# Kernel tuning notes

Hardware: AMD Instinct MI355X
Metric: run time of the kernel (lower is better)

## Reference

```python
import jax, jax.numpy as jnp
import numpy as np

EPS = 1e-5

def _act_quant(x, bits=8):
    # per-token absmax quantization to signed int range, dequantized (STE)
    qb = float(2 ** (bits - 1) - 1)  # 127 for 8 bits
    scale = qb / jnp.clip(jnp.max(jnp.abs(x), axis=-1, keepdims=True), EPS, None)
    x_dq = jnp.clip(jnp.round(x * scale), -qb, qb) / scale
    return x + jax.lax.stop_gradient(x_dq - x)

def _weight_quant(w):
    # BitNet b1.58 ternary weights: scale = mean |W|, values in {-1,0,1} * scale (STE)
    s = jnp.clip(jnp.mean(jnp.abs(w)), EPS, None)
    w_dq = jnp.clip(jnp.round(w / s), -1.0, 1.0) * s
    return w + jax.lax.stop_gradient(w_dq - w)

def _bitlinear(x, w, bits=8):
    # x: [..., in], w: [out, in]
    return jnp.einsum('bsi,oi->bso', _act_quant(x, bits), _weight_quant(w))

def setup_inputs() -> dict:
    key = jax.random.key(0)
    k1, k2, k3 = jax.random.split(key, 3)
    B, S, H = 4, 4096, 2048
    I = int(H * 2.0)
    return {
        'hidden_states': jax.random.normal(k1, (B, S, H), dtype=jnp.float32),
        'w_up': jax.random.normal(k2, (I, H), dtype=jnp.float32) * (1.0 / np.sqrt(H)),
        'w_down': jax.random.normal(k3, (H, I), dtype=jnp.float32) * (1.0 / np.sqrt(I)),
    }

def reference(hidden_states, w_up, w_down):
    bits = 8
    h = _bitlinear(hidden_states, w_up, bits)          # [B,S,I]
    h = jnp.square(jax.nn.relu(h))                      # squared ReLU
    # dropout p=0.0 (eval) -> identity
    out = _bitlinear(h, w_down, bits)                   # [B,S,H]
    return out
```

## Files before the change

kernel.cpp:

```cpp
#include <hip/hip_runtime.h>
#include <hip/hip_bf16.h>

typedef signed char i8_t;
typedef _Float16 half_t;
typedef float v4fl __attribute__((ext_vector_type(4)));
typedef _Float16 v8h __attribute__((ext_vector_type(8)));
typedef int v4i __attribute__((ext_vector_type(4)));
typedef signed char v8c __attribute__((ext_vector_type(8)));
typedef signed char v16c __attribute__((ext_vector_type(16)));

__device__ __forceinline__ float ternqf(float w, float s) {
    float q = rintf(w / s);
    return fminf(1.f, fmaxf(-1.f, q));
}

__device__ __forceinline__ void gload16(const void* g, void* l) {
    __builtin_amdgcn_global_load_lds(
        (const __attribute__((address_space(1))) void*)g,
        (__attribute__((address_space(3))) void*)l, 16, 0, 0);
}

__global__ void abssum_partial2(const float* __restrict__ wup,
                                const float* __restrict__ wdn, long n,
                                float* __restrict__ part_up,
                                float* __restrict__ part_dn) {
    const int half = gridDim.x >> 1;
    const bool up = (blockIdx.x < half);
    const float* w = up ? wup : wdn;
    float* partial = up ? part_up : part_dn;
    const int bid = up ? blockIdx.x : blockIdx.x - half;
    long i0 = ((long)bid * 256 + threadIdx.x) * 8;
    long stride = (long)half * 256 * 8;
    float s = 0.f;
    for (long i = i0; i < n; i += stride) {
        v4fl a = *(const v4fl*)(w + i);
        v4fl b = *(const v4fl*)(w + i + 4);
#pragma unroll
        for (int j = 0; j < 4; ++j) s += fabsf(a[j]) + fabsf(b[j]);
    }
#pragma unroll
    for (int off = 32; off > 0; off >>= 1) s += __shfl_down(s, off, 64);
    __shared__ __align__(16) float red[4];
    if ((threadIdx.x & 63) == 0) red[threadIdx.x >> 6] = s;
    __syncthreads();
    if (threadIdx.x == 0)
        partial[bid] = (red[0] + red[1]) + (red[2] + red[3]);
}

__global__ void abssum_final(const float* __restrict__ part_up,
                             const float* __restrict__ part_dn,
                             float* __restrict__ scales, float inv) {
    const int wv = threadIdx.x >> 6;
    const int l = threadIdx.x & 63;
    const float* part = wv ? part_dn : part_up;
    float s = ((part[l] + part[l + 64]) + (part[l + 128] + part[l + 192]));
#pragma unroll
    for (int off = 32; off > 0; off >>= 1) s += __shfl_down(s, off, 64);
    if (l == 0) scales[wv] = fmaxf(s * inv, 1e-5f);
}

__global__ void wquant2_kernel(const float* __restrict__ wup,
                               const float* __restrict__ wdn,
                               i8_t* __restrict__ wqu, i8_t* __restrict__ wqd,
                               const float* __restrict__ scales, int wblocks) {
    const bool up = ((int)blockIdx.x < wblocks);
    const float* w = up ? wup : wdn;
    i8_t* wq = up ? wqu : wqd;
    const float s = up ? scales[0] : scales[1];
    const int bid = up ? blockIdx.x : blockIdx.x - wblocks;
    long i = ((long)bid * 256 + threadIdx.x) * 8;
    v4fl a = *(const v4fl*)(w + i);
    v4fl b = *(const v4fl*)(w + i + 4);
    v8c o;
#pragma unroll
    for (int j = 0; j < 4; ++j) {
        o[j]     = (i8_t)(int)ternqf(a[j], s);
        o[j + 4] = (i8_t)(int)ternqf(b[j], s);
    }
    *(v8c*)(wq + i) = o;
}

template <int W>
__global__ void rowquant_kernel(const float* __restrict__ src, i8_t* __restrict__ dst,
                                float* __restrict__ scale_out, int rows) {
    const int l = threadIdx.x & 63;
    const int row = blockIdx.x * 4 + (threadIdx.x >> 6);
    if (row >= rows) return;
    const int NI = W / 1024;
    const float* p = src + (size_t)row * W + l * 16;
    float v[NI * 16];
#pragma unroll
    for (int it = 0; it < NI; ++it) {
#pragma unroll
        for (int c = 0; c < 4; ++c) {
            v4fl a = *(const v4fl*)(p + it * 1024 + c * 4);
#pragma unroll
            for (int e = 0; e < 4; ++e) v[it * 16 + c * 4 + e] = a[e];
        }
    }
    float amax = 0.f;
#pragma unroll
    for (int j = 0; j < NI * 16; ++j) amax = fmaxf(amax, fabsf(v[j]));
#pragma unroll
    for (int off = 32; off > 0; off >>= 1)
        amax = fmaxf(amax, __shfl_xor(amax, off, 64));
    const float m = fmaxf(amax, 1e-5f);
    if (l == 0) scale_out[row] = m / 127.f;
    const float sc = 127.f / m;
    i8_t* q = dst + (size_t)row * W + l * 16;
#pragma unroll
    for (int it = 0; it < NI; ++it) {
        v16c o;
#pragma unroll
        for (int j = 0; j < 16; ++j) {
            float t = rintf(v[it * 16 + j] * sc);
            o[j] = (i8_t)(int)fminf(127.f, fmaxf(-127.f, t));
        }
        *(v16c*)(q + it * 1024) = o;
    }
}

template <typename T, int NV>
__global__ void hamax_kernel(const T* __restrict__ h, float* __restrict__ scale_out,
                             float* __restrict__ recip_out) {
    const int row = blockIdx.x;
    const int tid = threadIdx.x;
    const T* p = h + (size_t)row * (NV * 2048);
    float amax = 0.f;
#pragma unroll
    for (int it = 0; it < NV; ++it) {
        const T* s = p + ((size_t)it * 256 + tid) * 8;
#pragma unroll
        for (int j = 0; j < 8; ++j) amax = fmaxf(amax, fabsf((float)s[j]));
    }
#pragma unroll
    for (int off = 32; off > 0; off >>= 1) amax = fmaxf(amax, __shfl_xor(amax, off, 64));
    __shared__ __align__(16) float red[4];
    if ((tid & 63) == 0) red[tid >> 6] = amax;
    __syncthreads();
    if (tid == 0) {
        float m = fmaxf(fmaxf(red[0], red[1]), fmaxf(red[2], red[3]));
        m = fmaxf(m, 1e-5f);
        scale_out[row] = m / 127.f;
        recip_out[row] = 127.f / m;
    }
}

__device__ __forceinline__ void stage_tile256(const i8_t* __restrict__ g, int K,
                                              i8_t* l, int tid) {
#pragma unroll
    for (int i = 0; i < 4; ++i) {
        const int c = i * 512 + tid;
        const int r = c >> 3;
        const int lc = (((c & 7) ^ (r & 7)) << 4);
        gload16(g + (size_t)r * K + lc, l + c * 16);
    }
}

#define SB() __builtin_amdgcn_sched_barrier(0)

template <int EPI>
__launch_bounds__(512, 2)
__global__ void gemm_bt8(const i8_t* __restrict__ A, const i8_t* __restrict__ B,
                         void* __restrict__ Cv,
                         const float* __restrict__ rowscale,
                         const float* __restrict__ wscale,
                         int M, int N, int K) {
    __shared__ __align__(16) i8_t smem[131072];

    const int tid = threadIdx.x;

    const int gx = gridDim.x;
    const int nwg = gx * gridDim.y;
    int flat = blockIdx.y * gx + blockIdx.x;
    if ((nwg & 7) == 0) flat = (flat & 7) * (nwg >> 3) + (flat >> 3);
    const int n0 = (flat % gx) * 256;
    const int m0 = (flat / gx) * 256;

    const i8_t* gA = A + (size_t)m0 * K;
    const i8_t* gB = B + (size_t)n0 * K;

    const int w = tid >> 6, l = tid & 63;
    const int wr = w >> 2, wc = w & 3;
    const int lrow = l & 15, lq = l >> 4;
    const int lr7 = lrow & 7;
    const int kk0 = ((lq)     ^ lr7) << 4;
    const int kk1 = ((lq + 4) ^ lr7) << 4;
    const int aBase = ((wr * 128 + lrow) << 7);
    const int bBase = ((wc * 64 + lrow) << 7);

    v4i acc[8][4];
#pragma unroll
    for (int a = 0; a < 8; ++a)
#pragma unroll
        for (int b = 0; b < 4; ++b) acc[a][b] = (v4i){0, 0, 0, 0};

    const int NT = K >> 7;
    stage_tile256(gB, K, smem + 32768, tid);
    stage_tile256(gA, K, smem, tid);
    stage_tile256(gB + 128, K, smem + 65536 + 32768, tid);
    stage_tile256(gA + 128, K, smem + 65536, tid);
    asm volatile("s_waitcnt vmcnt(8)" ::: "memory");
    __builtin_amdgcn_s_barrier();
    SB();

    for (int t = 0; t < NT; ++t) {
        i8_t* Ab = smem + ((t & 1) << 16);
        i8_t* Bb = Ab + 32768;
        const bool pf = (t + 2 < NT);

        v4i a0[4], a1[4], b0[4], b1[4];

#pragma unroll
        for (int nj = 0; nj < 4; ++nj)
            b0[nj] = *(const v4i*)(Bb + bBase + (nj << 11) + kk0);
#pragma unroll
        for (int mi = 0; mi < 4; ++mi)
            a0[mi] = *(const v4i*)(Ab + aBase + (mi << 11) + kk0);
        SB();
#pragma unroll
        for (int nj = 0; nj < 4; ++nj)
            b1[nj] = *(const v4i*)(Bb + bBase + (nj << 11) + kk1);
#pragma unroll
        for (int mi = 0; mi < 4; ++mi)
            a1[mi] = *(const v4i*)(Ab + aBase + ((mi + 4) << 11) + kk0);
        SB();
        asm volatile("s_waitcnt lgkmcnt(8)" ::: "memory");
        SB();
        __builtin_amdgcn_s_setprio(1);
#pragma unroll
        for (int mi = 0; mi < 4; ++mi)
#pragma unroll
            for (int nj = 0; nj < 4; ++nj)
                acc[mi][nj] = __builtin_amdgcn_mfma_i32_16x16x64_i8(
                    a0[mi], b0[nj], acc[mi][nj], 0, 0, 0);
        __builtin_amdgcn_s_setprio(0);
        SB();
#pragma unroll
        for (int mi = 0; mi < 4; ++mi)
            a0[mi] = *(const v4i*)(Ab + aBase + (mi << 11) + kk1);
        SB();
        asm volatile("s_waitcnt lgkmcnt(4)" ::: "memory");
        SB();
        __builtin_amdgcn_s_setprio(1);
#pragma unroll
        for (int mi = 0; mi < 4; ++mi)
#pragma unroll
            for (int nj = 0; nj < 4; ++nj)
                acc[mi + 4][nj] = __builtin_amdgcn_mfma_i32_16x16x64_i8(
                    a1[mi], b0[nj], acc[mi + 4][nj], 0, 0, 0);
        __builtin_amdgcn_s_setprio(0);
        SB();
#pragma unroll
        for (int mi = 0; mi < 4; ++mi)
            a1[mi] = *(const v4i*)(Ab + aBase + ((mi + 4) << 11) + kk1);
        SB();
        asm volatile("s_waitcnt lgkmcnt(0)" ::: "memory");
        SB();
        __builtin_amdgcn_s_barrier();
        SB();
        if (pf) {
            stage_tile256(gB + (size_t)(t + 2) * 128, K, Bb, tid);
            stage_tile256(gA + (size_t)(t + 2) * 128, K, Ab, tid);
        }
        SB();
        __builtin_amdgcn_s_setprio(1);
#pragma unroll
        for (int mi = 0; mi < 4; ++mi)
#pragma unroll
            for (int nj = 0; nj < 4; ++nj)
                acc[mi][nj] = __builtin_amdgcn_mfma_i32_16x16x64_i8(
                    a0[mi], b1[nj], acc[mi][nj], 0, 0, 0);
#pragma unroll
        for (int mi = 0; mi < 4; ++mi)
#pragma unroll
            for (int nj = 0; nj < 4; ++nj)
                acc[mi + 4][nj] = __builtin_amdgcn_mfma_i32_16x16x64_i8(
                    a1[mi], b1[nj], acc[mi + 4][nj], 0, 0, 0);
        __builtin_amdgcn_s_setprio(0);
        SB();
        if (pf) {
            asm volatile("s_waitcnt vmcnt(8)" ::: "memory");
        } else if (t + 1 < NT) {
            asm volatile("s_waitcnt vmcnt(0)" ::: "memory");
        }
        if (t + 1 < NT) {
            __builtin_amdgcn_s_barrier();
            SB();
        }
    }

    const float sw = wscale[0];
#pragma unroll
    for (int mi = 0; mi < 8; ++mi) {
#pragma unroll
        for (int r = 0; r < 4; ++r) {
            const int row = m0 + wr * 128 + mi * 16 + lq * 4 + r;
            const float rs = sw * rowscale[row];
#pragma unroll
            for (int nj = 0; nj < 4; ++nj) {
                const int col = n0 + wc * 64 + nj * 16 + lrow;
                float v = (float)acc[mi][nj][r] * rs;
                if (EPI == 0) {
                    ((float*)Cv)[(size_t)row * N + col] = v;
                } else {
                    v = fmaxf(v, 0.f); v = v * v;
                    ((float*)Cv)[(size_t)row * N + col] = v;
                }
            }
        }
    }
}

template <int ASRC, int EPI>
__launch_bounds__(256, 2)
__global__ void gemm_bt(const void* __restrict__ Av, const i8_t* __restrict__ B,
                        void* __restrict__ Cv,
                        const float* __restrict__ rowscale,
                        const float* __restrict__ arecip,
                        const float* __restrict__ wscale,
                        int M, int N, int K) {
    __shared__ __align__(16) i8_t As[128 * 64];
    __shared__ __align__(16) i8_t Bs[128 * 64];

    const int tid = threadIdx.x;
    const int gx = gridDim.x;
    const int nwg = gx * gridDim.y;
    int flat = blockIdx.y * gx + blockIdx.x;
    if ((nwg & 7) == 0) flat = (flat & 7) * (nwg >> 3) + (flat >> 3);
    const int n0 = (flat % gx) * 128;
    const int m0 = (flat / gx) * 128;

    const int srow = tid >> 2;
    const int scol = (tid & 3) * 16;
    const i8_t* gB0 = B + (size_t)(n0 + srow) * K + scol;
    const i8_t* gB1 = B + (size_t)(n0 + 64 + srow) * K + scol;
    i8_t* lB0 = Bs + tid * 16;
    i8_t* lB1 = Bs + 4096 + tid * 16;

    const i8_t* gA0 = nullptr;
    const i8_t* gA1 = nullptr;
    i8_t* lA0 = As + tid * 16;
    i8_t* lA1 = As + 4096 + tid * 16;
    if (ASRC == 0) {
        gA0 = (const i8_t*)Av + (size_t)(m0 + srow) * K + scol;
        gA1 = (const i8_t*)Av + (size_t)(m0 + 64 + srow) * K + scol;
    }

    const int qrow = tid >> 1;
    const int qcol = (tid & 1) * 32;
    const float* gA32 = (const float*)Av + (size_t)(m0 + qrow) * K + qcol;
    const half_t* gAh = (const half_t*)Av + (size_t)(m0 + qrow) * K + qcol;
    i8_t* qdst = As + qrow * 64 + qcol;
    const float qsc = (ASRC != 0) ? arecip[m0 + qrow] : 0.f;

    const int w = tid >> 6, l = tid & 63;
    const int wr = w >> 1, wc = w & 1;
    const int lrow = l & 15, lq = l >> 4;

    v4i acc[4][4];
#pragma unroll
    for (int a = 0; a < 4; ++a)
#pragma unroll
        for (int b = 0; b < 4; ++b) acc[a][b] = (v4i){0, 0, 0, 0};

    const int kiters = K / 64;
    for (int kt = 0; kt < kiters; ++kt) {
        const int off = kt * 64;
        v16c r0, r1;
        if (ASRC == 1) {
#pragma unroll
            for (int c = 0; c < 4; ++c) {
                v4fl f0 = *(const v4fl*)(gA32 + off + c * 4);
                v4fl f1 = *(const v4fl*)(gA32 + off + 16 + c * 4);
#pragma unroll
                for (int e = 0; e < 4; ++e) {
                    float t0 = rintf(f0[e] * qsc);
                    float t1 = rintf(f1[e] * qsc);
                    r0[c * 4 + e] = (i8_t)(int)fminf(127.f, fmaxf(-127.f, t0));
                    r1[c * 4 + e] = (i8_t)(int)fminf(127.f, fmaxf(-127.f, t1));
                }
            }
        } else if (ASRC == 2) {
#pragma unroll
            for (int c = 0; c < 2; ++c) {
                v8h h0 = *(const v8h*)(gAh + off + c * 8);
                v8h h1 = *(const v8h*)(gAh + off + 16 + c * 8);
#pragma unroll
                for (int e = 0; e < 8; ++e) {
                    float t0 = rintf((float)h0[e] * qsc);
                    float t1 = rintf((float)h1[e] * qsc);
                    r0[c * 8 + e] = (i8_t)(int)fminf(127.f, fmaxf(-127.f, t0));
                    r1[c * 8 + e] = (i8_t)(int)fminf(127.f, fmaxf(-127.f, t1));
                }
            }
        }
        __syncthreads();
        gload16(gB0 + off, lB0);
        gload16(gB1 + off, lB1);
        if (ASRC == 0) {
            gload16(gA0 + off, lA0);
            gload16(gA1 + off, lA1);
        } else {
            *(v16c*)qdst = r0;
            *(v16c*)(qdst + 16) = r1;
        }
        __syncthreads();

        v4i af[4], bfr[4];
#pragma unroll
        for (int mi = 0; mi < 4; ++mi)
            af[mi] = *(const v4i*)(As + (wr * 64 + mi * 16 + lrow) * 64 + lq * 16);
#pragma unroll
        for (int nj = 0; nj < 4; ++nj)
            bfr[nj] = *(const v4i*)(Bs + (wc * 64 + nj * 16 + lrow) * 64 + lq * 16);
#pragma unroll
        for (int mi = 0; mi < 4; ++mi)
#pragma unroll
            for (int nj = 0; nj < 4; ++nj)
                acc[mi][nj] = __builtin_amdgcn_mfma_i32_16x16x64_i8(
                    af[mi], bfr[nj], acc[mi][nj], 0, 0, 0);
    }

    const float sw = wscale[0];
#pragma unroll
    for (int mi = 0; mi < 4; ++mi) {
#pragma unroll
        for (int r = 0; r < 4; ++r) {
            const int row = m0 + wr * 64 + mi * 16 + lq * 4 + r;
            const float rs = sw * rowscale[row];
#pragma unroll
            for (int nj = 0; nj < 4; ++nj) {
                const int col = n0 + wc * 64 + nj * 16 + lrow;
                float v = (float)acc[mi][nj][r] * rs;
                if (EPI == 0) {
                    ((float*)Cv)[(size_t)row * N + col] = v;
                } else if (EPI == 1) {
                    v = fmaxf(v, 0.f); v = v * v;
                    ((half_t*)Cv)[(size_t)row * N + col] = (half_t)v;
                } else {
                    v = fmaxf(v, 0.f); v = v * v;
                    ((float*)Cv)[(size_t)row * N + col] = v;
                }
            }
        }
    }
}

extern "C" void kernel_launch(void* const* d_in, const int* in_sizes, int n_in,
                              void* d_out, int out_size, void* d_ws, size_t ws_size,
                              hipStream_t stream) {
    const float* x   = (const float*)d_in[0];
    const float* wup = (const float*)d_in[1];
    const float* wdn = (const float*)d_in[2];

    const int H = 2048;
    const int T = in_sizes[0] / H;
    const int I = in_sizes[1] / H;
    const long nw = (long)in_sizes[1];
    const float winv = 1.0f / (float)nw;

    char* p = (char*)d_ws;
    float* scales  = (float*)p;
    float* part_up = (float*)(p + 256);
    float* part_dn = (float*)(p + 1280);
    float* a_scale = (float*)(p + 2304);
    float* h_scale = a_scale + T;
    float* h_recip = h_scale + T;
    size_t off = 2304 + (size_t)12 * T;
    off = (off + 255) & ~(size_t)255;
    i8_t* xq  = (i8_t*)(p + off); off += (size_t)T * H;
    off = (off + 255) & ~(size_t)255;
    i8_t* wqu = (i8_t*)(p + off); off += (size_t)I * H;
    off = (off + 255) & ~(size_t)255;
    i8_t* wqd = (i8_t*)(p + off); off += (size_t)H * I;
    off = (off + 255) & ~(size_t)255;
    void* h  = (void*)(p + off);
    i8_t* hq = (i8_t*)(p + off + (size_t)T * I * 4);

    const size_t need_full = off + (size_t)T * I * 5;
    const size_t need_h32  = off + (size_t)T * I * 4;
    const int mode = (ws_size == 0 || need_full <= ws_size) ? 0
                   : (need_h32 <= ws_size ? 1 : 2);
    const bool big_ok = (T % 256 == 0) && (I % 256 == 0) && (H % 256 == 0) &&
                        (H >= 256) && (I >= 256);

    abssum_partial2<<<512, 256, 0, stream>>>(wup, wdn, nw, part_up, part_dn);
    abssum_final<<<1, 128, 0, stream>>>(part_up, part_dn, scales, winv);

    int wblocks = (int)(nw / 2048);
    wquant2_kernel<<<2 * wblocks, 256, 0, stream>>>(wup, wdn, wqu, wqd, scales, wblocks);

    rowquant_kernel<2048><<<(T + 3) / 4, 256, 0, stream>>>(x, xq, a_scale, T);

    if (mode == 0 && big_ok) {
        gemm_bt8<2><<<dim3(I / 256, T / 256), 512, 0, stream>>>(
            xq, wqu, h, a_scale, scales + 0, T, I, H);
        rowquant_kernel<4096><<<(T + 3) / 4, 256, 0, stream>>>(
            (const float*)h, hq, h_scale, T);
        gemm_bt8<0><<<dim3(H / 256, T / 256), 512, 0, stream>>>(
            hq, wqd, d_out, h_scale, scales + 1, T, H, I);
    } else if (mode == 0) {
        gemm_bt<0, 2><<<dim3(I / 128, T / 128), 256, 0, stream>>>(
            xq, wqu, h, a_scale, nullptr, scales + 0, T, I, H);
        rowquant_kernel<4096><<<(T + 3) / 4, 256, 0, stream>>>(
            (const float*)h, hq, h_scale, T);
        gemm_bt<0, 0><<<dim3(H / 128, T / 128), 256, 0, stream>>>(
            hq, wqd, d_out, h_scale, nullptr, scales + 1, T, H, I);
    } else if (mode == 1) {
        gemm_bt<0, 2><<<dim3(I / 128, T / 128), 256, 0, stream>>>(
            xq, wqu, h, a_scale, nullptr, scales + 0, T, I, H);
        hamax_kernel<float, 2><<<T, 256, 0, stream>>>((const float*)h, h_scale, h_recip);
        gemm_bt<1, 0><<<dim3(H / 128, T / 128), 256, 0, stream>>>(
            h, wqd, d_out, h_scale, h_recip, scales + 1, T, H, I);
    } else {
        gemm_bt<0, 1><<<dim3(I / 128, T / 128), 256, 0, stream>>>(
            xq, wqu, h, a_scale, nullptr, scales + 0, T, I, H);
        hamax_kernel<half_t, 2><<<T, 256, 0, stream>>>((const half_t*)h, h_scale, h_recip);
        gemm_bt<2, 0><<<dim3(H / 128, T / 128), 256, 0, stream>>>(
            h, wqd, d_out, h_scale, h_recip, scales + 1, T, H, I);
    }
}
```

Measured before the change: 614.2 us.

## Switch int8 GEMM to BK=64 triple-buffered LDS pipeline with early prefetch

The K-tile shrinks from 128 to 64 bytes, and the LDS ring goes from two to three stages (96KB instead of 128KB). Global-to-LDS prefetch for tile t+2 is issued at the top of each iteration, so there is no mid-iteration barrier before restaging. The XOR swizzle is rewritten for 64-byte rows. This halves the MFMA work per barrier, which adds relative sync overhead, and it risks more LDS bank conflicts with the new swizzle.

```diff
diff --git a/kernel.cpp b/kernel.cpp
--- a/kernel.cpp
+++ b/kernel.cpp
@@ -146,14 +146,15 @@
     }
 }
 
-__device__ __forceinline__ void stage_tile256(const i8_t* __restrict__ g, int K,
+__device__ __forceinline__ void stage_tile64b(const i8_t* __restrict__ g, int K,
                                               i8_t* l, int tid) {
 #pragma unroll
-    for (int i = 0; i < 4; ++i) {
+    for (int i = 0; i < 2; ++i) {
         const int c = i * 512 + tid;
-        const int r = c >> 3;
-        const int lc = (((c & 7) ^ (r & 7)) << 4);
-        gload16(g + (size_t)r * K + lc, l + c * 16);
+        const int r = c >> 2;
+        const int s = c & 3;
+        const int gc = ((s ^ ((r >> 1) & 3)) << 4);
+        gload16(g + (size_t)r * K + gc, l + c * 16);
     }
 }
 
@@ -166,7 +167,7 @@
                          const float* __restrict__ rowscale,
                          const float* __restrict__ wscale,
                          int M, int N, int K) {
-    __shared__ __align__(16) i8_t smem[131072];
+    __shared__ __align__(16) i8_t smem[98304];
 
     const int tid = threadIdx.x;
 
@@ -183,11 +184,9 @@
     const int w = tid >> 6, l = tid & 63;
     const int wr = w >> 2, wc = w & 3;
     const int lrow = l & 15, lq = l >> 4;
-    const int lr7 = lrow & 7;
-    const int kk0 = ((lq)     ^ lr7) << 4;
-    const int kk1 = ((lq + 4) ^ lr7) << 4;
-    const int aBase = ((wr * 128 + lrow) << 7);
-    const int bBase = ((wc * 64 + lrow) << 7);
+    const int koff = ((lq ^ ((lrow >> 1) & 3)) << 4);
+    const int aBase = ((wr * 128 + lrow) << 6) + koff;
+    const int bBase = ((wc * 64 + lrow) << 6) + koff;
 
     v4i acc[8][4];
 #pragma unroll
@@ -195,37 +194,42 @@
 #pragma unroll
         for (int b = 0; b < 4; ++b) acc[a][b] = (v4i){0, 0, 0, 0};
 
-    const int NT = K >> 7;
-    stage_tile256(gB, K, smem + 32768, tid);
-    stage_tile256(gA, K, smem, tid);
-    stage_tile256(gB + 128, K, smem + 65536 + 32768, tid);
-    stage_tile256(gA + 128, K, smem + 65536, tid);
-    asm volatile("s_waitcnt vmcnt(8)" ::: "memory");
+    const int NT = K >> 6;
+    stage_tile64b(gB, K, smem + 16384, tid);
+    stage_tile64b(gA, K, smem, tid);
+    stage_tile64b(gB + 64, K, smem + 32768 + 16384, tid);
+    stage_tile64b(gA + 64, K, smem + 32768, tid);
+    asm volatile("s_waitcnt vmcnt(4)" ::: "memory");
     __builtin_amdgcn_s_barrier();
     SB();
 
+    int cur = 0;
     for (int t = 0; t < NT; ++t) {
-        i8_t* Ab = smem + ((t & 1) << 16);
-        i8_t* Bb = Ab + 32768;
+        i8_t* Ab = smem + cur * 32768;
+        i8_t* Bb = Ab + 16384;
         const bool pf = (t + 2 < NT);
 
-        v4i a0[4], a1[4], b0[4], b1[4];
-
+        if (pf) {
+            int s2 = cur + 2; if (s2 >= 3) s2 -= 3;
+            i8_t* Sb = smem + s2 * 32768;
+            stage_tile64b(gB + (size_t)(t + 2) * 64, K, Sb + 16384, tid);
+            stage_tile64b(gA + (size_t)(t + 2) * 64, K, Sb, tid);
+        }
+        SB();
+
+        v4i a0[4], a1[4], b0[4];
 #pragma unroll
         for (int nj = 0; nj < 4; ++nj)
-            b0[nj] = *(const v4i*)(Bb + bBase + (nj << 11) + kk0);
-#pragma unroll
-        for (int mi = 0; mi < 4; ++mi)
-            a0[mi] = *(const v4i*)(Ab + aBase + (mi << 11) + kk0);
-        SB();
-#pragma unroll
-        for (int nj = 0; nj < 4; ++nj)
-            b1[nj] = *(const v4i*)(Bb + bBase + (nj << 11) + kk1);
-#pragma unroll
-        for (int mi = 0; mi < 4; ++mi)
-            a1[mi] = *(const v4i*)(Ab + aBase + ((mi + 4) << 11) + kk0);
-        SB();
-        asm volatile("s_waitcnt lgkmcnt(8)" ::: "memory");
+            b0[nj] = *(const v4i*)(Bb + bBase + (nj << 10));
+#pragma unroll
+        for (int mi = 0; mi < 4; ++mi)
+            a0[mi] = *(const v4i*)(Ab + aBase + (mi << 10));
+        SB();
+#pragma unroll
+        for (int mi = 0; mi < 4; ++mi)
+            a1[mi] = *(const v4i*)(Ab + aBase + ((mi + 4) << 10));
+        SB();
+        asm volatile("s_waitcnt lgkmcnt(4)" ::: "memory");
         SB();
         __builtin_amdgcn_s_setprio(1);
 #pragma unroll
@@ -236,11 +240,7 @@
                     a0[mi], b0[nj], acc[mi][nj], 0, 0, 0);
         __builtin_amdgcn_s_setprio(0);
         SB();
-#pragma unroll
-        for (int mi = 0; mi < 4; ++mi)
-            a0[mi] = *(const v4i*)(Ab + aBase + (mi << 11) + kk1);
-        SB();
-        asm volatile("s_waitcnt lgkmcnt(4)" ::: "memory");
+        asm volatile("s_waitcnt lgkmcnt(0)" ::: "memory");
         SB();
         __builtin_amdgcn_s_setprio(1);
 #pragma unroll
@@ -251,36 +251,8 @@
                     a1[mi], b0[nj], acc[mi + 4][nj], 0, 0, 0);
         __builtin_amdgcn_s_setprio(0);
         SB();
-#pragma unroll
-        for (int mi = 0; mi < 4; ++mi)
-            a1[mi] = *(const v4i*)(Ab + aBase + ((mi + 4) << 11) + kk1);
-        SB();
-        asm volatile("s_waitcnt lgkmcnt(0)" ::: "memory");
-        SB();
-        __builtin_amdgcn_s_barrier();
-        SB();
         if (pf) {
-            stage_tile256(gB + (size_t)(t + 2) * 128, K, Bb, tid);
-            stage_tile256(gA + (size_t)(t + 2) * 128, K, Ab, tid);
-        }
-        SB();
-        __builtin_amdgcn_s_setprio(1);
-#pragma unroll
-        for (int mi = 0; mi < 4; ++mi)
-#pragma unroll
-            for (int nj = 0; nj < 4; ++nj)
-                acc[mi][nj] = __builtin_amdgcn_mfma_i32_16x16x64_i8(
-                    a0[mi], b1[nj], acc[mi][nj], 0, 0, 0);
-#pragma unroll
-        for (int mi = 0; mi < 4; ++mi)
-#pragma unroll
-            for (int nj = 0; nj < 4; ++nj)
-                acc[mi + 4][nj] = __builtin_amdgcn_mfma_i32_16x16x64_i8(
-                    a1[mi], b1[nj], acc[mi + 4][nj], 0, 0, 0);
-        __builtin_amdgcn_s_setprio(0);
-        SB();
-        if (pf) {
-            asm volatile("s_waitcnt vmcnt(8)" ::: "memory");
+            asm volatile("s_waitcnt vmcnt(4)" ::: "memory");
         } else if (t + 1 < NT) {
             asm volatile("s_waitcnt vmcnt(0)" ::: "memory");
         }
@@ -288,6 +260,7 @@
             __builtin_amdgcn_s_barrier();
             SB();
         }
+        ++cur; if (cur == 3) cur = 0;
     }
 
     const float sw = wscale[0];
```

Result: no change. 622.8 us (+1.4%).
